# Performance work log

Measured on AMD Instinct MI355X. Metric: run time of the kernel, lower is better.

## Reference

```python
import jax, jax.numpy as jnp
import numpy as np

N_NODES = 100000
N_EDGES = 1600000
D = 32
K = 3  # Chebyshev kernels
NEG_SLOPE = 0.2


def setup_inputs() -> dict:
    key = jax.random.key(0)
    ks = jax.random.split(key, 10)
    s = 1.0 / np.sqrt(D)
    return {
        "u": jax.random.normal(ks[0], (N_NODES, D), jnp.float32),
        "lambda_max": jnp.full((1,), 2.0, jnp.float32),
        "edge_src": jax.random.randint(ks[1], (N_EDGES,), 0, N_NODES, jnp.int32),
        "edge_dst": jax.random.randint(ks[2], (N_EDGES,), 0, N_NODES, jnp.int32),
        "cheb_W": jax.random.normal(ks[3], (K * D, D), jnp.float32) * s,
        "cheb_b": jnp.zeros((D,), jnp.float32),
        "src_W": jax.random.normal(ks[4], (D, D), jnp.float32) * s,
        "src_b": jnp.zeros((D,), jnp.float32),
        "dst_W": jax.random.normal(ks[5], (D, D), jnp.float32) * s,
        "dst_b": jnp.zeros((D,), jnp.float32),
        "attn": jax.random.normal(ks[6], (1, D), jnp.float32) * s,  # (heads=1, D)
    }


def reference(u, lambda_max, edge_src, edge_dst, cheb_W, cheb_b,
              src_W, src_b, dst_W, dst_b, attn):
    N = u.shape[0]
    # in-degrees (DGL: clamp(min=1) ** -0.5)
    deg = jnp.zeros((N,), u.dtype).at[edge_dst].add(1.0)
    Dinv = jnp.clip(deg, 1.0, None) ** -0.5  # (N,)

    def unnL(x):  # D^{-1/2} A D^{-1/2} x  via copy_u->sum message passing
        m = (x * Dinv[:, None])[edge_src]                       # (E, D)
        agg = jax.ops.segment_sum(m, edge_dst, num_segments=N)  # (N, D)
        return agg * Dinv[:, None]

    # --- ChebConv ---
    re_norm = 2.0 / lambda_max  # (1,) broadcast over all nodes
    X0 = u
    Xt = [X0]
    X1 = X0
    if K > 1:
        h = unnL(X0)
        X1 = -re_norm * h + X0 * (re_norm - 1.0)
        Xt.append(X1)
    for _ in range(2, K):
        h = unnL(X1)
        Xi = -2.0 * re_norm * h + X1 * (2.0 * (re_norm - 1.0)) - X0
        Xt.append(Xi)
        X0, X1 = X1, Xi
    Xcat = jnp.concatenate(Xt, axis=1)                 # (N, K*D)
    hc = jax.nn.relu(Xcat @ cheb_W + cheb_b)           # (N, D), DGL default activation=relu

    # --- GATv2Conv (heads=1) ---
    H = attn.shape[0]
    fsrc = (hc @ src_W + src_b).reshape(N, H, -1)      # (N, H, D)
    fdst = (hc @ dst_W + dst_b).reshape(N, H, -1)
    e = jax.nn.leaky_relu(fsrc[edge_src] + fdst[edge_dst], NEG_SLOPE)  # (E, H, D)
    logits = jnp.einsum('ehd,hd->eh', e, attn)         # (E, H)
    mx = jax.ops.segment_max(logits, edge_dst, num_segments=N)
    mx = jnp.where(jnp.isfinite(mx), mx, 0.0)
    ex = jnp.exp(logits - mx[edge_dst])
    den = jax.ops.segment_sum(ex, edge_dst, num_segments=N)
    a = ex / jnp.where(den > 0, den, 1.0)[edge_dst]    # edge softmax over dst groups
    msg = fsrc[edge_src] * a[:, :, None]               # (E, H, D)
    out = jax.ops.segment_sum(msg, edge_dst, num_segments=N)  # (N, H, D)
    return out.squeeze(1)
```

## Files before the change

### kernel.cpp

```cpp
#include <hip/hip_runtime.h>
#include <hip/hip_bf16.h>


typedef unsigned short u16;

#define DD 32
#define NEG_SLOPE 0.2f
#define BLK 256
#define TILE 8192
#define CB_SHIFT 9
#define CB_NODES 512
#define SRC_BITS 17

#define OFF_CHEBW 0
#define OFF_CHEBB 3072
#define OFF_SRCW  3104
#define OFF_SRCB  4128
#define OFF_DSTW  4160
#define OFF_DSTB  5184
#define OFF_ATTN  5216
#define OFF_LMAX  5248
#define W_TOTAL   5249

#define F_U     0
#define F_CHEBW 1
#define F_CHEBB 2
#define F_SRCW  3
#define F_SRCB  4
#define F_DSTW  5
#define F_DSTB  6
#define F_ATTN  7
#define F_LMAX  8
#define N_FLAGS 9

__device__ __forceinline__ float bh2f(u16 h) {
    return __uint_as_float(((unsigned)h) << 16);
}
__device__ __forceinline__ float rdin(const void* p, long long i, int f32f) {
    return f32f ? ((const float*)p)[i] : bh2f(((const u16*)p)[i]);
}
__device__ __forceinline__ float4 rd4(const void* p, long long row, int q, int f32f) {
    if (f32f) return ((const float4*)p)[row * 8 + q];
    ushort4 h = ((const ushort4*)p)[row * 8 + q];
    return make_float4(bh2f(h.x), bh2f(h.y), bh2f(h.z), bh2f(h.w));
}
__device__ __forceinline__ float lrelu(float x) { return fmaxf(x, NEG_SLOPE * x); }

__device__ __forceinline__ int plaus(u16 h) {
    if ((h & 0x7FFFu) == 0) return 1;
    unsigned e = (h >> 7) & 0xFF;
    return (e >= 0x60 && e <= 0x8F) ? 1 : 0;
}

__global__ void k_detect(const void* p0, const void* p1, const void* p2,
                         const void* p3, const void* p4, const void* p5,
                         const void* p6, const void* p7, const void* p8,
                         int n0, int n7, int* __restrict__ flags) {
    __shared__ int cEven, cEvenZ, cOddNZ;
    const void* ptrs[N_FLAGS] = {p0, p1, p2, p3, p4, p5, p6, p7, p8};
    const int   ns[N_FLAGS]   = {n0, 3072, 32, 1024, 32, 1024, 32, n7, 1};
    int a = blockIdx.x;
    if (a >= N_FLAGS) return;
    const u16* h = (const u16*)ptrs[a];
    int n = ns[a];
    if (threadIdx.x == 0) { cEven = 0; cEvenZ = 0; cOddNZ = 0; }
    __syncthreads();
    if (n == 1) {
        if (threadIdx.x == 0) {
            u16 v = h[0];
            flags[a] = ((v & 0x7FFFu) == 0 || !plaus(v)) ? 1 : 0;
        }
        return;
    }
    int nprobe = n >> 1;
    if (nprobe > 64) nprobe = 64;
    int t = threadIdx.x;
    if (t < nprobe) {
        u16 ev = h[2 * t];
        u16 od = h[2 * t + 1];
        if (plaus(ev)) atomicAdd(&cEven, 1);
        if ((ev & 0x7FFFu) == 0) atomicAdd(&cEvenZ, 1);
        if (plaus(od) && (od & 0x7FFFu) != 0) atomicAdd(&cOddNZ, 1);
    }
    __syncthreads();
    if (threadIdx.x == 0) {
        int bf = (cEven * 4 >= nprobe * 3);
        if (cEvenZ == nprobe && cOddNZ * 2 >= nprobe) bf = 0;
        flags[a] = bf ? 0 : 1;
    }
}

__global__ void k_cvtw(const void* chebW, const void* chebB, const void* srcW,
                       const void* srcB, const void* dstW, const void* dstB,
                       const void* attn, const void* lmax,
                       const int* __restrict__ flags, float* __restrict__ wsW) {
    int i = blockIdx.x * blockDim.x + threadIdx.x;
    if (i >= W_TOTAL) return;
    float v;
    if      (i < OFF_CHEBB) v = rdin(chebW, i - OFF_CHEBW, flags[F_CHEBW]);
    else if (i < OFF_SRCW)  v = rdin(chebB, i - OFF_CHEBB, flags[F_CHEBB]);
    else if (i < OFF_SRCB)  v = rdin(srcW,  i - OFF_SRCW,  flags[F_SRCW]);
    else if (i < OFF_DSTW)  v = rdin(srcB,  i - OFF_SRCB,  flags[F_SRCB]);
    else if (i < OFF_DSTB)  v = rdin(dstW,  i - OFF_DSTW,  flags[F_DSTW]);
    else if (i < OFF_ATTN)  v = rdin(dstB,  i - OFF_DSTB,  flags[F_DSTB]);
    else if (i < OFF_LMAX)  v = rdin(attn,  i - OFF_ATTN,  flags[F_ATTN]);
    else                    v = rdin(lmax,  0,             flags[F_LMAX]);
    wsW[i] = v;
}


__global__ __launch_bounds__(BLK) void k_h1(
        const int* __restrict__ dst, unsigned* __restrict__ hist1,
        int E, int T, int NB1) {
    __shared__ unsigned lh[256];
    int tile = blockIdx.x, t = threadIdx.x;
    lh[t] = 0;
    __syncthreads();
    int base = tile * TILE;
    for (int i = 0; i < TILE / BLK; i++) {
        int e = base + i * BLK + t;
        if (e < E) atomicAdd(&lh[dst[e] >> CB_SHIFT], 1u);
    }
    __syncthreads();
    for (int b = t; b < NB1; b += BLK) hist1[(size_t)b * T + tile] = lh[b];
}

__global__ __launch_bounds__(BLK) void k_scA(
        unsigned* __restrict__ h, unsigned* __restrict__ bsum, int T) {
    __shared__ unsigned s[BLK];
    int b = blockIdx.x, t = threadIdx.x;
    unsigned carry = 0;
    for (int base = 0; base < T; base += BLK) {
        int i = base + t;
        unsigned v = (i < T) ? h[(size_t)b * T + i] : 0u;
        s[t] = v;
        __syncthreads();
        for (int off = 1; off < BLK; off <<= 1) {
            unsigned a = (t >= off) ? s[t - off] : 0u;
            __syncthreads();
            s[t] += a;
            __syncthreads();
        }
        if (i < T) h[(size_t)b * T + i] = carry + s[t] - v;
        carry += s[BLK - 1];
        __syncthreads();
    }
    if (t == 0) bsum[b] = carry;
}

__global__ __launch_bounds__(BLK) void k_scB(
        unsigned* __restrict__ bsum, int NB1,
        unsigned* __restrict__ row_ptr, int N, int E) {
    __shared__ unsigned s[BLK];
    int t = threadIdx.x;
    unsigned v = (t < NB1) ? bsum[t] : 0u;
    s[t] = v;
    __syncthreads();
    for (int off = 1; off < BLK; off <<= 1) {
        unsigned a = (t >= off) ? s[t - off] : 0u;
        __syncthreads();
        s[t] += a;
        __syncthreads();
    }
    if (t < NB1) bsum[t] = s[t] - v;
    if (t == 0) row_ptr[N] = (unsigned)E;
}

__global__ __launch_bounds__(BLK) void k_s1(
        const int* __restrict__ src, const int* __restrict__ dst,
        const unsigned* __restrict__ off1, const unsigned* __restrict__ bsum,
        unsigned* __restrict__ tmp, int E, int T, int NB1) {
    __shared__ unsigned cur[256];
    int tile = blockIdx.x, t = threadIdx.x;
    for (int b = t; b < NB1; b += BLK)
        cur[b] = off1[(size_t)b * T + tile] + bsum[b];
    __syncthreads();
    int base = tile * TILE;
    for (int i = 0; i < TILE / BLK; i++) {
        int e = base + i * BLK + t;
        if (e < E) {
            int d = dst[e];
            unsigned pos = atomicAdd(&cur[d >> CB_SHIFT], 1u);
            tmp[pos] = ((unsigned)(d & (CB_NODES - 1)) << SRC_BITS) | (unsigned)src[e];
        }
    }
}

__global__ __launch_bounds__(BLK) void k_p2(
        const unsigned* __restrict__ tmp, const unsigned* __restrict__ bsum,
        unsigned* __restrict__ row_ptr, float* __restrict__ dinv,
        int* __restrict__ srcs, int N, int E, int T, int NB1) {
    __shared__ unsigned hist[CB_NODES], offs[CB_NODES], cur[CB_NODES], ssc[BLK];
    int b = blockIdx.x, t = threadIdx.x;
    int nodeBase = b << CB_SHIFT;
    unsigned lo = bsum[b];
    unsigned hi = (b + 1 < NB1) ? bsum[b + 1] : (unsigned)E;
    hist[t] = 0; hist[t + BLK] = 0;
    __syncthreads();
    for (unsigned e = lo + t; e < hi; e += BLK)
        atomicAdd(&hist[tmp[e] >> SRC_BITS], 1u);
    __syncthreads();
    unsigned a0 = hist[2 * t], a1 = hist[2 * t + 1];
    unsigned ps = a0 + a1;
    ssc[t] = ps;
    __syncthreads();
    for (int off = 1; off < BLK; off <<= 1) {
        unsigned a = (t >= off) ? ssc[t - off] : 0u;
        __syncthreads();
        ssc[t] += a;
        __syncthreads();
    }
    unsigned pbase = ssc[t] - ps;
    offs[2 * t] = pbase;
    offs[2 * t + 1] = pbase + a0;
    cur[2 * t] = pbase;
    cur[2 * t + 1] = pbase + a0;
    for (int k = 0; k < 2; k++) {
        int i = 2 * t + k;
        int node = nodeBase + i;
        if (node < N) {
            row_ptr[node] = lo + offs[i];
            unsigned c = hist[i];
            if (c < 1u) c = 1u;
            dinv[node] = rsqrtf((float)c);
        }
    }
    __syncthreads();
    for (unsigned e = lo + t; e < hi; e += BLK) {
        unsigned p = tmp[e];
        unsigned pos = lo + atomicAdd(&cur[p >> SRC_BITS], 1u);
        srcs[pos] = (int)(p & ((1u << SRC_BITS) - 1u));
    }
}


__global__ __launch_bounds__(BLK) void k_unnl1(
        const void* __restrict__ u, const int* __restrict__ flags,
        const float* __restrict__ dinv, const unsigned* __restrict__ row_ptr,
        const int* __restrict__ srcs, const float* __restrict__ wsW,
        float* __restrict__ X1, int N) {
    int wave = (blockIdx.x * BLK + threadIdx.x) >> 6;
    if (wave >= N) return;
    int lane = threadIdx.x & 63, q = lane & 7, g = lane >> 3;
    int f = flags[F_U];
    int base = (int)row_ptr[wave], end = (int)row_ptr[wave + 1];
    float4 acc = make_float4(0.f, 0.f, 0.f, 0.f);
    for (int i = base; i < end; i += 16) {
        int e0 = i + g, e1 = i + 8 + g;
        int ec0 = min(e0, end - 1), ec1 = min(e1, end - 1);
        int s0 = srcs[ec0], s1 = srcs[ec1];
        float dv0 = dinv[s0], dv1 = dinv[s1];
        if (e0 >= end) dv0 = 0.f;
        if (e1 >= end) dv1 = 0.f;
        float4 x0 = rd4(u, s0, q, f);
        float4 x1 = rd4(u, s1, q, f);
        acc.x += x0.x * dv0 + x1.x * dv1;
        acc.y += x0.y * dv0 + x1.y * dv1;
        acc.z += x0.z * dv0 + x1.z * dv1;
        acc.w += x0.w * dv0 + x1.w * dv1;
    }
#pragma unroll
    for (int off = 8; off <= 32; off <<= 1) {
        acc.x += __shfl_xor(acc.x, off);
        acc.y += __shfl_xor(acc.y, off);
        acc.z += __shfl_xor(acc.z, off);
        acc.w += __shfl_xor(acc.w, off);
    }
    if (g == 0) {
        float rn = 2.0f / wsW[OFF_LMAX];
        float dn = dinv[wave];
        float4 x0 = rd4(u, wave, q, f);
        float4 r;
        r.x = -rn * (acc.x * dn) + x0.x * (rn - 1.f);
        r.y = -rn * (acc.y * dn) + x0.y * (rn - 1.f);
        r.z = -rn * (acc.z * dn) + x0.z * (rn - 1.f);
        r.w = -rn * (acc.w * dn) + x0.w * (rn - 1.f);
        ((float4*)X1)[(size_t)wave * 8 + q] = r;
    }
}

__global__ __launch_bounds__(BLK) void k_unnl2(
        const void* __restrict__ u, const int* __restrict__ flags,
        const float* __restrict__ X1, const float* __restrict__ dinv,
        const unsigned* __restrict__ row_ptr, const int* __restrict__ srcs,
        const float* __restrict__ wsW, float* __restrict__ X2, int N) {
    int wave = (blockIdx.x * BLK + threadIdx.x) >> 6;
    if (wave >= N) return;
    int lane = threadIdx.x & 63, q = lane & 7, g = lane >> 3;
    int base = (int)row_ptr[wave], end = (int)row_ptr[wave + 1];
    float4 acc = make_float4(0.f, 0.f, 0.f, 0.f);
    for (int i = base; i < end; i += 16) {
        int e0 = i + g, e1 = i + 8 + g;
        int ec0 = min(e0, end - 1), ec1 = min(e1, end - 1);
        int s0 = srcs[ec0], s1 = srcs[ec1];
        float dv0 = dinv[s0], dv1 = dinv[s1];
        if (e0 >= end) dv0 = 0.f;
        if (e1 >= end) dv1 = 0.f;
        float4 x0 = ((const float4*)X1)[(size_t)s0 * 8 + q];
        float4 x1 = ((const float4*)X1)[(size_t)s1 * 8 + q];
        acc.x += x0.x * dv0 + x1.x * dv1;
        acc.y += x0.y * dv0 + x1.y * dv1;
        acc.z += x0.z * dv0 + x1.z * dv1;
        acc.w += x0.w * dv0 + x1.w * dv1;
    }
#pragma unroll
    for (int off = 8; off <= 32; off <<= 1) {
        acc.x += __shfl_xor(acc.x, off);
        acc.y += __shfl_xor(acc.y, off);
        acc.z += __shfl_xor(acc.z, off);
        acc.w += __shfl_xor(acc.w, off);
    }
    if (g == 0) {
        float rn = 2.0f / wsW[OFF_LMAX];
        float dn = dinv[wave];
        float4 x0 = rd4(u, wave, q, flags[F_U]);
        float4 x1 = ((const float4*)X1)[(size_t)wave * 8 + q];
        float4 r;
        r.x = -2.f * rn * (acc.x * dn) + x1.x * (2.f * (rn - 1.f)) - x0.x;
        r.y = -2.f * rn * (acc.y * dn) + x1.y * (2.f * (rn - 1.f)) - x0.y;
        r.z = -2.f * rn * (acc.z * dn) + x1.z * (2.f * (rn - 1.f)) - x0.z;
        r.w = -2.f * rn * (acc.w * dn) + x1.w * (2.f * (rn - 1.f)) - x0.w;
        ((float4*)X2)[(size_t)wave * 8 + q] = r;
    }
}

__global__ __launch_bounds__(BLK) void k_cfsd(
        const void* __restrict__ u, const int* __restrict__ flags,
        const float* __restrict__ X1, const float* __restrict__ X2,
        const float* __restrict__ wsW, float* __restrict__ fsrc,
        float* __restrict__ fdst, unsigned* __restrict__ Mabs, int N) {
    __shared__ float sW[3072], sWs[1024], sWd[1024];
    __shared__ float sb[32], sbs[32], sbd[32];
    __shared__ float hcS[BLK * 33];
    __shared__ unsigned mloc[32];
    int t = threadIdx.x;
    for (int i = t; i < 3072; i += BLK) sW[i] = wsW[OFF_CHEBW + i];
    for (int i = t; i < 1024; i += BLK) {
        sWs[i] = wsW[OFF_SRCW + i];
        sWd[i] = wsW[OFF_DSTW + i];
    }
    if (t < 32) {
        sb[t]  = wsW[OFF_CHEBB + t];
        sbs[t] = wsW[OFF_SRCB + t];
        sbd[t] = wsW[OFF_DSTB + t];
        mloc[t] = 0u;
    }
    __syncthreads();
    int f = flags[F_U];
    float mabs = 0.f;
    int n = blockIdx.x * BLK + t;
    if (n < N) {
        long long row = (long long)n;
        float acc[32];
#pragma unroll
        for (int j = 0; j < 32; j++) acc[j] = sb[j];
        for (int i4 = 0; i4 < 8; i4++) {
            float4 x = rd4(u, row, i4, f);
            const float* w = &sW[i4 * 128];
#pragma unroll
            for (int j = 0; j < 32; j++) acc[j] = fmaf(x.x, w[j], acc[j]);
#pragma unroll
            for (int j = 0; j < 32; j++) acc[j] = fmaf(x.y, w[32 + j], acc[j]);
#pragma unroll
            for (int j = 0; j < 32; j++) acc[j] = fmaf(x.z, w[64 + j], acc[j]);
#pragma unroll
            for (int j = 0; j < 32; j++) acc[j] = fmaf(x.w, w[96 + j], acc[j]);
        }
        for (int i4 = 0; i4 < 8; i4++) {
            float4 x = ((const float4*)X1)[row * 8 + i4];
            const float* w = &sW[1024 + i4 * 128];
#pragma unroll
            for (int j = 0; j < 32; j++) acc[j] = fmaf(x.x, w[j], acc[j]);
#pragma unroll
            for (int j = 0; j < 32; j++) acc[j] = fmaf(x.y, w[32 + j], acc[j]);
#pragma unroll
            for (int j = 0; j < 32; j++) acc[j] = fmaf(x.z, w[64 + j], acc[j]);
#pragma unroll
            for (int j = 0; j < 32; j++) acc[j] = fmaf(x.w, w[96 + j], acc[j]);
        }
        for (int i4 = 0; i4 < 8; i4++) {
            float4 x = ((const float4*)X2)[row * 8 + i4];
            const float* w = &sW[2048 + i4 * 128];
#pragma unroll
            for (int j = 0; j < 32; j++) acc[j] = fmaf(x.x, w[j], acc[j]);
#pragma unroll
            for (int j = 0; j < 32; j++) acc[j] = fmaf(x.y, w[32 + j], acc[j]);
#pragma unroll
            for (int j = 0; j < 32; j++) acc[j] = fmaf(x.z, w[64 + j], acc[j]);
#pragma unroll
            for (int j = 0; j < 32; j++) acc[j] = fmaf(x.w, w[96 + j], acc[j]);
        }
#pragma unroll
        for (int j = 0; j < 32; j++) hcS[t * 33 + j] = fmaxf(acc[j], 0.f);
        float as[32], ad[32];
#pragma unroll
        for (int j = 0; j < 32; j++) { as[j] = sbs[j]; ad[j] = sbd[j]; }
        for (int i = 0; i < 32; i++) {
            float hv = hcS[t * 33 + i];
            const float* ws = &sWs[i * 32];
            const float* wd = &sWd[i * 32];
#pragma unroll
            for (int j = 0; j < 32; j++) {
                as[j] = fmaf(hv, ws[j], as[j]);
                ad[j] = fmaf(hv, wd[j], ad[j]);
            }
        }
        float4* fs4 = (float4*)(fsrc + row * 32);
        float4* fd4 = (float4*)(fdst + row * 32);
#pragma unroll
        for (int i4 = 0; i4 < 8; i4++) {
            fs4[i4] = make_float4(as[4 * i4], as[4 * i4 + 1], as[4 * i4 + 2], as[4 * i4 + 3]);
            fd4[i4] = make_float4(ad[4 * i4], ad[4 * i4 + 1], ad[4 * i4 + 2], ad[4 * i4 + 3]);
        }
#pragma unroll
        for (int j = 0; j < 32; j++) mabs = fmaxf(mabs, fabsf(as[j]));
    }
    atomicMax(&mloc[t & 31], __float_as_uint(mabs));
    __syncthreads();
    if (t < 32) atomicMax(&Mabs[t], mloc[t]);
}

__global__ __launch_bounds__(BLK) void k_gat(
        const float* __restrict__ fsrc, const float* __restrict__ fdst,
        const unsigned* __restrict__ row_ptr, const int* __restrict__ srcs,
        const float* __restrict__ wsW, const unsigned* __restrict__ Mabs,
        float* __restrict__ out, int N) {
    int wave = (blockIdx.x * BLK + threadIdx.x) >> 6;
    if (wave >= N) return;
    int lane = threadIdx.x & 63, q = lane & 7, g = lane >> 3;
    int base = (int)row_ptr[wave], end = (int)row_ptr[wave + 1];
    if (base == end) {
        if (g == 0)
            ((float4*)out)[(size_t)wave * 8 + q] = make_float4(0.f, 0.f, 0.f, 0.f);
        return;
    }
    float4 fd = ((const float4*)fdst)[(size_t)wave * 8 + q];
    float4 at = ((const float4*)(wsW + OFF_ATTN))[q];
    float4 mb = ((const float4*)Mabs)[q];
    float kp = (mb.x + fabsf(fd.x)) * fabsf(at.x) +
               (mb.y + fabsf(fd.y)) * fabsf(at.y) +
               (mb.z + fabsf(fd.z)) * fabsf(at.z) +
               (mb.w + fabsf(fd.w)) * fabsf(at.w);
    kp += __shfl_xor(kp, 1);
    kp += __shfl_xor(kp, 2);
    kp += __shfl_xor(kp, 4);
    float K = kp;
    float4 acc = make_float4(0.f, 0.f, 0.f, 0.f);
    float den = 0.f;
    for (int i = base; i < end; i += 16) {
        int e0 = i + g, e1 = i + 8 + g;
        int ec0 = min(e0, end - 1), ec1 = min(e1, end - 1);
        int s0 = srcs[ec0], s1 = srcs[ec1];
        float4 fs0 = ((const float4*)fsrc)[(size_t)s0 * 8 + q];
        float4 fs1 = ((const float4*)fsrc)[(size_t)s1 * 8 + q];
        float v0 = lrelu(fs0.x + fd.x) * at.x + lrelu(fs0.y + fd.y) * at.y +
                   lrelu(fs0.z + fd.z) * at.z + lrelu(fs0.w + fd.w) * at.w;
        float v1 = lrelu(fs1.x + fd.x) * at.x + lrelu(fs1.y + fd.y) * at.y +
                   lrelu(fs1.z + fd.z) * at.z + lrelu(fs1.w + fd.w) * at.w;
        v0 += __shfl_xor(v0, 1);  v1 += __shfl_xor(v1, 1);
        v0 += __shfl_xor(v0, 2);  v1 += __shfl_xor(v1, 2);
        v0 += __shfl_xor(v0, 4);  v1 += __shfl_xor(v1, 4);
        float w0 = (e0 < end) ? __expf(v0 - K) : 0.f;
        float w1 = (e1 < end) ? __expf(v1 - K) : 0.f;
        acc.x += fs0.x * w0 + fs1.x * w1;
        acc.y += fs0.y * w0 + fs1.y * w1;
        acc.z += fs0.z * w0 + fs1.z * w1;
        acc.w += fs0.w * w0 + fs1.w * w1;
        den += w0 + w1;
    }
#pragma unroll
    for (int off = 8; off <= 32; off <<= 1) {
        acc.x += __shfl_xor(acc.x, off);
        acc.y += __shfl_xor(acc.y, off);
        acc.z += __shfl_xor(acc.z, off);
        acc.w += __shfl_xor(acc.w, off);
        den   += __shfl_xor(den, off);
    }
    if (g == 0) {
        float inv = 1.f / (den > 0.f ? den : 1.f);
        ((float4*)out)[(size_t)wave * 8 + q] =
            make_float4(acc.x * inv, acc.y * inv, acc.z * inv, acc.w * inv);
    }
}

extern "C" void kernel_launch(void* const* d_in, const int* in_sizes, int n_in,
                              void* d_out, int out_size, void* d_ws, size_t ws_size,
                              hipStream_t stream) {
    const void* u     = d_in[0];
    const void* lmax  = d_in[1];
    const int*  esrc  = (const int*)d_in[2];
    const int*  edst  = (const int*)d_in[3];
    const void* chebW = d_in[4];
    const void* chebB = d_in[5];
    const void* srcW  = d_in[6];
    const void* srcB  = d_in[7];
    const void* dstW  = d_in[8];
    const void* dstB  = d_in[9];
    const void* attn  = d_in[10];

    const int ND = in_sizes[0];
    const int N  = ND / DD;
    const int E  = in_sizes[2];

    const int NB1 = (N + CB_NODES - 1) >> CB_SHIFT;
    const int T   = (E + TILE - 1) / TILE;
    const int M   = NB1 * T;

    float* ws   = (float*)d_ws;
    float* X1   = ws;
    float* X2   = ws + (size_t)ND;
    unsigned* tmp = (unsigned*)(ws + 2 * (size_t)ND);
    int*   srcs = (int*)(tmp + E);
    unsigned* hist1   = (unsigned*)(srcs + E);
    unsigned* row_ptr = hist1 + M;
    float*    dinv    = (float*)(row_ptr + (N + 1));
    unsigned* bsum    = (unsigned*)(dinv + N);
    float*    wsW     = (float*)(((uintptr_t)(bsum + NB1) + 15) & ~(uintptr_t)15);
    int*      flags   = (int*)(wsW + W_TOTAL);
    unsigned* Mabs    = (unsigned*)(((uintptr_t)(flags + N_FLAGS) + 15) & ~(uintptr_t)15);
    float*    out     = (float*)d_out;

    auto gb = [](long long n, int b) { return (unsigned)((n + b - 1) / b); };

    k_detect<<<N_FLAGS, 64, 0, stream>>>(u, chebW, chebB, srcW, srcB, dstW, dstB,
                                         attn, lmax, ND, DD, flags);
    k_cvtw<<<gb(W_TOTAL, BLK), BLK, 0, stream>>>(chebW, chebB, srcW, srcB, dstW, dstB,
                                                 attn, lmax, flags, wsW);
    hipMemsetAsync(Mabs, 0, 32 * sizeof(unsigned), stream);

    k_h1<<<T, BLK, 0, stream>>>(edst, hist1, E, T, NB1);
    k_scA<<<NB1, BLK, 0, stream>>>(hist1, bsum, T);
    k_scB<<<1, BLK, 0, stream>>>(bsum, NB1, row_ptr, N, E);
    k_s1<<<T, BLK, 0, stream>>>(esrc, edst, hist1, bsum, tmp, E, T, NB1);
    k_p2<<<NB1, BLK, 0, stream>>>(tmp, bsum, row_ptr, dinv, srcs, N, E, T, NB1);

    k_unnl1<<<gb((long long)N * 64, BLK), BLK, 0, stream>>>(u, flags, dinv, row_ptr,
                                                            srcs, wsW, X1, N);
    k_unnl2<<<gb((long long)N * 64, BLK), BLK, 0, stream>>>(u, flags, X1, dinv, row_ptr,
                                                            srcs, wsW, X2, N);

    k_cfsd<<<gb(N, BLK), BLK, 0, stream>>>(u, flags, X1, X2, wsW, X1, X2, Mabs, N);

    k_gat<<<gb((long long)N * 64, BLK), BLK, 0, stream>>>(X1, X2, row_ptr, srcs,
                                                          wsW, Mabs, out, N);
}
```

Before: 303.6 us.

## Shrink sort buckets, fold Mabs memset into weight kernel, unroll gathers 4x

Bucket width for the two-pass CSR build drops from 512 to 256 nodes, and the tile size for the histogram and scatter passes is halved. This doubles the number of buckets and tiles, giving more blocks in the second pass, and the per-bucket scan now maps one node per thread. The memset of the Mabs accumulator moves into the weight-conversion kernel, which removes one API call. The Chebyshev aggregation loops now process four edges per lane group per iteration instead of two, putting more loads in flight at the cost of extra registers and more wasted work on low-degree nodes.

```diff
diff --git a/kernel.cpp b/kernel.cpp
--- a/kernel.cpp
+++ b/kernel.cpp
@@ -7,9 +7,9 @@
 #define DD 32
 #define NEG_SLOPE 0.2f
 #define BLK 256
-#define TILE 8192
-#define CB_SHIFT 9
-#define CB_NODES 512
+#define TILE 4096
+#define CB_SHIFT 8
+#define CB_NODES 256
 #define SRC_BITS 17
 
 #define OFF_CHEBW 0
@@ -93,9 +93,11 @@
 __global__ void k_cvtw(const void* chebW, const void* chebB, const void* srcW,
                        const void* srcB, const void* dstW, const void* dstB,
                        const void* attn, const void* lmax,
-                       const int* __restrict__ flags, float* __restrict__ wsW) {
+                       const int* __restrict__ flags, float* __restrict__ wsW,
+                       unsigned* __restrict__ Mabs) {
     int i = blockIdx.x * blockDim.x + threadIdx.x;
-    if (i >= W_TOTAL) return;
+    if (i >= W_TOTAL + 32) return;
+    if (i >= W_TOTAL) { Mabs[i - W_TOTAL] = 0u; return; }
     float v;
     if      (i < OFF_CHEBB) v = rdin(chebW, i - OFF_CHEBW, flags[F_CHEBW]);
     else if (i < OFF_SRCW)  v = rdin(chebB, i - OFF_CHEBB, flags[F_CHEBB]);
@@ -112,9 +114,9 @@
 __global__ __launch_bounds__(BLK) void k_h1(
         const int* __restrict__ dst, unsigned* __restrict__ hist1,
         int E, int T, int NB1) {
-    __shared__ unsigned lh[256];
+    __shared__ unsigned lh[512];
     int tile = blockIdx.x, t = threadIdx.x;
-    lh[t] = 0;
+    for (int b = t; b < 512; b += BLK) lh[b] = 0;
     __syncthreads();
     int base = tile * TILE;
     for (int i = 0; i < TILE / BLK; i++) {
@@ -148,15 +150,15 @@
     if (t == 0) bsum[b] = carry;
 }
 
-__global__ __launch_bounds__(BLK) void k_scB(
+__global__ __launch_bounds__(512) void k_scB(
         unsigned* __restrict__ bsum, int NB1,
         unsigned* __restrict__ row_ptr, int N, int E) {
-    __shared__ unsigned s[BLK];
+    __shared__ unsigned s[512];
     int t = threadIdx.x;
     unsigned v = (t < NB1) ? bsum[t] : 0u;
     s[t] = v;
     __syncthreads();
-    for (int off = 1; off < BLK; off <<= 1) {
+    for (int off = 1; off < 512; off <<= 1) {
         unsigned a = (t >= off) ? s[t - off] : 0u;
         __syncthreads();
         s[t] += a;
@@ -170,7 +172,7 @@
         const int* __restrict__ src, const int* __restrict__ dst,
         const unsigned* __restrict__ off1, const unsigned* __restrict__ bsum,
         unsigned* __restrict__ tmp, int E, int T, int NB1) {
-    __shared__ unsigned cur[256];
+    __shared__ unsigned cur[512];
     int tile = blockIdx.x, t = threadIdx.x;
     for (int b = t; b < NB1; b += BLK)
         cur[b] = off1[(size_t)b * T + tile] + bsum[b];
@@ -190,19 +192,18 @@
         const unsigned* __restrict__ tmp, const unsigned* __restrict__ bsum,
         unsigned* __restrict__ row_ptr, float* __restrict__ dinv,
         int* __restrict__ srcs, int N, int E, int T, int NB1) {
-    __shared__ unsigned hist[CB_NODES], offs[CB_NODES], cur[CB_NODES], ssc[BLK];
+    __shared__ unsigned hist[CB_NODES], cur[CB_NODES], ssc[BLK];
     int b = blockIdx.x, t = threadIdx.x;
     int nodeBase = b << CB_SHIFT;
     unsigned lo = bsum[b];
     unsigned hi = (b + 1 < NB1) ? bsum[b + 1] : (unsigned)E;
-    hist[t] = 0; hist[t + BLK] = 0;
+    hist[t] = 0;
     __syncthreads();
     for (unsigned e = lo + t; e < hi; e += BLK)
         atomicAdd(&hist[tmp[e] >> SRC_BITS], 1u);
     __syncthreads();
-    unsigned a0 = hist[2 * t], a1 = hist[2 * t + 1];
-    unsigned ps = a0 + a1;
-    ssc[t] = ps;
+    unsigned v = hist[t];
+    ssc[t] = v;
     __syncthreads();
     for (int off = 1; off < BLK; off <<= 1) {
         unsigned a = (t >= off) ? ssc[t - off] : 0u;
@@ -210,20 +211,14 @@
         ssc[t] += a;
         __syncthreads();
     }
-    unsigned pbase = ssc[t] - ps;
-    offs[2 * t] = pbase;
-    offs[2 * t + 1] = pbase + a0;
-    cur[2 * t] = pbase;
-    cur[2 * t + 1] = pbase + a0;
-    for (int k = 0; k < 2; k++) {
-        int i = 2 * t + k;
-        int node = nodeBase + i;
-        if (node < N) {
-            row_ptr[node] = lo + offs[i];
-            unsigned c = hist[i];
-            if (c < 1u) c = 1u;
-            dinv[node] = rsqrtf((float)c);
-        }
+    unsigned ex = ssc[t] - v;
+    cur[t] = ex;
+    int node = nodeBase + t;
+    if (node < N) {
+        row_ptr[node] = lo + ex;
+        unsigned c = v;
+        if (c < 1u) c = 1u;
+        dinv[node] = rsqrtf((float)c);
     }
     __syncthreads();
     for (unsigned e = lo + t; e < hi; e += BLK) {
@@ -245,19 +240,23 @@
     int f = flags[F_U];
     int base = (int)row_ptr[wave], end = (int)row_ptr[wave + 1];
     float4 acc = make_float4(0.f, 0.f, 0.f, 0.f);
-    for (int i = base; i < end; i += 16) {
-        int e0 = i + g, e1 = i + 8 + g;
-        int ec0 = min(e0, end - 1), ec1 = min(e1, end - 1);
-        int s0 = srcs[ec0], s1 = srcs[ec1];
-        float dv0 = dinv[s0], dv1 = dinv[s1];
+    for (int i = base; i < end; i += 32) {
+        int e0 = i + g, e1 = i + 8 + g, e2 = i + 16 + g, e3 = i + 24 + g;
+        int s0 = srcs[min(e0, end - 1)], s1 = srcs[min(e1, end - 1)];
+        int s2 = srcs[min(e2, end - 1)], s3 = srcs[min(e3, end - 1)];
+        float dv0 = dinv[s0], dv1 = dinv[s1], dv2 = dinv[s2], dv3 = dinv[s3];
         if (e0 >= end) dv0 = 0.f;
         if (e1 >= end) dv1 = 0.f;
+        if (e2 >= end) dv2 = 0.f;
+        if (e3 >= end) dv3 = 0.f;
         float4 x0 = rd4(u, s0, q, f);
         float4 x1 = rd4(u, s1, q, f);
-        acc.x += x0.x * dv0 + x1.x * dv1;
-        acc.y += x0.y * dv0 + x1.y * dv1;
-        acc.z += x0.z * dv0 + x1.z * dv1;
-        acc.w += x0.w * dv0 + x1.w * dv1;
+        float4 x2 = rd4(u, s2, q, f);
+        float4 x3 = rd4(u, s3, q, f);
+        acc.x += x0.x * dv0 + x1.x * dv1 + x2.x * dv2 + x3.x * dv3;
+        acc.y += x0.y * dv0 + x1.y * dv1 + x2.y * dv2 + x3.y * dv3;
+        acc.z += x0.z * dv0 + x1.z * dv1 + x2.z * dv2 + x3.z * dv3;
+        acc.w += x0.w * dv0 + x1.w * dv1 + x2.w * dv2 + x3.w * dv3;
     }
 #pragma unroll
     for (int off = 8; off <= 32; off <<= 1) {
@@ -289,19 +288,23 @@
     int lane = threadIdx.x & 63, q = lane & 7, g = lane >> 3;
     int base = (int)row_ptr[wave], end = (int)row_ptr[wave + 1];
     float4 acc = make_float4(0.f, 0.f, 0.f, 0.f);
-    for (int i = base; i < end; i += 16) {
-        int e0 = i + g, e1 = i + 8 + g;
-        int ec0 = min(e0, end - 1), ec1 = min(e1, end - 1);
-        int s0 = srcs[ec0], s1 = srcs[ec1];
-        float dv0 = dinv[s0], dv1 = dinv[s1];
+    for (int i = base; i < end; i += 32) {
+        int e0 = i + g, e1 = i + 8 + g, e2 = i + 16 + g, e3 = i + 24 + g;
+        int s0 = srcs[min(e0, end - 1)], s1 = srcs[min(e1, end - 1)];
+        int s2 = srcs[min(e2, end - 1)], s3 = srcs[min(e3, end - 1)];
+        float dv0 = dinv[s0], dv1 = dinv[s1], dv2 = dinv[s2], dv3 = dinv[s3];
         if (e0 >= end) dv0 = 0.f;
         if (e1 >= end) dv1 = 0.f;
+        if (e2 >= end) dv2 = 0.f;
+        if (e3 >= end) dv3 = 0.f;
         float4 x0 = ((const float4*)X1)[(size_t)s0 * 8 + q];
         float4 x1 = ((const float4*)X1)[(size_t)s1 * 8 + q];
-        acc.x += x0.x * dv0 + x1.x * dv1;
-        acc.y += x0.y * dv0 + x1.y * dv1;
-        acc.z += x0.z * dv0 + x1.z * dv1;
-        acc.w += x0.w * dv0 + x1.w * dv1;
+        float4 x2 = ((const float4*)X1)[(size_t)s2 * 8 + q];
+        float4 x3 = ((const float4*)X1)[(size_t)s3 * 8 + q];
+        acc.x += x0.x * dv0 + x1.x * dv1 + x2.x * dv2 + x3.x * dv3;
+        acc.y += x0.y * dv0 + x1.y * dv1 + x2.y * dv2 + x3.y * dv3;
+        acc.z += x0.z * dv0 + x1.z * dv1 + x2.z * dv2 + x3.z * dv3;
+        acc.w += x0.w * dv0 + x1.w * dv1 + x2.w * dv2 + x3.w * dv3;
     }
 #pragma unroll
     for (int off = 8; off <= 32; off <<= 1) {
@@ -524,13 +527,13 @@
 
     k_detect<<<N_FLAGS, 64, 0, stream>>>(u, chebW, chebB, srcW, srcB, dstW, dstB,
                                          attn, lmax, ND, DD, flags);
-    k_cvtw<<<gb(W_TOTAL, BLK), BLK, 0, stream>>>(chebW, chebB, srcW, srcB, dstW, dstB,
-                                                 attn, lmax, flags, wsW);
-    hipMemsetAsync(Mabs, 0, 32 * sizeof(unsigned), stream);
+    k_cvtw<<<gb(W_TOTAL + 32, BLK), BLK, 0, stream>>>(chebW, chebB, srcW, srcB,
+                                                      dstW, dstB, attn, lmax,
+                                                      flags, wsW, Mabs);
 
     k_h1<<<T, BLK, 0, stream>>>(edst, hist1, E, T, NB1);
     k_scA<<<NB1, BLK, 0, stream>>>(hist1, bsum, T);
-    k_scB<<<1, BLK, 0, stream>>>(bsum, NB1, row_ptr, N, E);
+    k_scB<<<1, 512, 0, stream>>>(bsum, NB1, row_ptr, N, E);
     k_s1<<<T, BLK, 0, stream>>>(esrc, edst, hist1, bsum, tmp, E, T, NB1);
     k_p2<<<NB1, BLK, 0, stream>>>(tmp, bsum, row_ptr, dinv, srcs, N, E, T, NB1);
 
```

Result: faster. 285.5 us (-5.9%).
